# Kernel tuning notes

Measured on AMD Instinct MI355X. Metric: run time of the kernel, lower is better.

## Reference

```python
import jax, jax.numpy as jnp
import numpy as np

B, T, H = 8, 4096, 1024
K, V = 128, 128
OUT = 1024

def setup_inputs() -> dict:
    key = jax.random.key(0)
    k1, k2, k3, k4, k5 = jax.random.split(key, 5)
    s = 1.0 / np.sqrt(H)
    return {
        "hidden_state": jax.random.normal(k1, (B, T, H), dtype=jnp.float32),
        "W_proj": jax.random.normal(k2, (H, 3 * K + V), dtype=jnp.float32) * s,
        "b_proj": jax.random.normal(k3, (3 * K + V,), dtype=jnp.float32) * 0.01,
        "W_out": jax.random.normal(k4, (V, OUT), dtype=jnp.float32) * (1.0 / np.sqrt(V)),
        "b_out": jax.random.normal(k5, (OUT,), dtype=jnp.float32) * 0.01,
    }

def reference(hidden_state, W_proj, b_proj, W_out, b_out):
    # fused projection over all timesteps at once: (B,T,3K+V)
    qkgv = jnp.einsum("bth,hd->btd", hidden_state, W_proj) + b_proj
    q, k, g, v = jnp.split(qkgv, [K, 2 * K, 3 * K], axis=-1)
    k = jax.nn.sigmoid(k)
    g = jax.nn.sigmoid(g)

    # time-major for scan: (T,B,*)
    xs = (jnp.swapaxes(q, 0, 1), jnp.swapaxes(k, 0, 1),
          jnp.swapaxes(g, 0, 1), jnp.swapaxes(v, 0, 1))
    cell0 = jnp.zeros((B, K, V), dtype=hidden_state.dtype)

    def step(cell, x):
        q_i, k_i, g_i, v_i = x
        # gated outer-product state update: cell (B,K,V)
        cell = cell * g_i[:, :, None] + k_i[:, :, None] * v_i[:, None, :]
        # query readout: (B,V)
        o_i = jnp.einsum("bkv,bk->bv", cell, q_i)
        return cell, o_i

    final_state, outs = jax.lax.scan(step, cell0, xs)
    outputs = jnp.swapaxes(outs, 0, 1)  # (B,T,V)
    outputs = jnp.einsum("btv,vo->bto", outputs, W_out) + b_out
    return outputs, final_state
```

## Files before the change

### kernel.cpp

```cpp
#include <hip/hip_runtime.h>
#include <math.h>

#define B_ 8
#define T_ 4096
#define H_ 1024
#define K_ 128
#define V_ 128
#define OUT_ 1024
#define NPROJ 512
#define M_ (B_*T_)
#define CC 32
#define NC 128

typedef __attribute__((ext_vector_type(8))) short bf16x8;
typedef __attribute__((ext_vector_type(4))) float f32x4;

__device__ inline unsigned short f2bf(float f){
  union{float f; unsigned int u;} x; x.f = f;
  unsigned int r = x.u + 0x7fff + ((x.u>>16)&1);
  return (unsigned short)(r>>16);
}
__device__ inline float bf2f(unsigned short u){
  union{unsigned int i; float f;} x; x.i = ((unsigned int)u)<<16; return x.f;
}

#define GL16(gp, lp) __builtin_amdgcn_global_load_lds(\
  (const __attribute__((address_space(1))) unsigned int*)(gp), \
  (__attribute__((address_space(3))) unsigned int*)(lp), 16, 0, 0)

#define MFMA16(a,b,c) __builtin_amdgcn_mfma_f32_16x16x32_bf16((a),(b),(c),0,0,0)

__global__ __launch_bounds__(256)
void convT(const float* __restrict__ src, unsigned short* __restrict__ dst,
           int Kd, int N) {
  __shared__ float t[32][33];
  int tx = threadIdx.x & 31, ty = threadIdx.x >> 5;
  int n0 = blockIdx.x * 32, k0 = blockIdx.y * 32;
  #pragma unroll
  for (int r=0;r<4;r++){
    int k = ty*4 + r;
    t[k][tx] = src[(long)(k0+k)*N + n0 + tx];
  }
  __syncthreads();
  #pragma unroll
  for (int r=0;r<4;r++){
    int n = ty*4 + r;
    dst[(long)(n0+n)*Kd + k0 + tx] = f2bf(t[tx][n]);
  }
}

__global__ __launch_bounds__(512)
void proj_mfma3(const float* __restrict__ A, const unsigned short* __restrict__ Bt,
                const float* __restrict__ bias,
                unsigned short* __restrict__ qbf, unsigned short* __restrict__ kbf,
                float* __restrict__ gf, unsigned short* __restrict__ vbf) {
  __shared__ unsigned short sA[2][128*32];
  __shared__ unsigned short sB[2][256*32];
  int tid = threadIdx.x, lane = tid & 63, wid = tid >> 6;
  int wm = wid >> 2, wn = wid & 3;
  int l16 = lane & 15, g8 = (lane >> 4) * 8;
  long row0 = (long)blockIdx.y * 128;
  int col0 = blockIdx.x * 256;

  int arow = tid >> 2, akoff = (tid & 3) * 8;
  const float* Ab = A + (row0 + arow) * 1024 + akoff;
  int srow = lane >> 2, soff = (lane & 3) * 8;

  f32x4 acc[4][4];
  #pragma unroll
  for (int i=0;i<4;i++)
    #pragma unroll
    for (int j=0;j<4;j++) acc[i][j] = (f32x4){0.f,0.f,0.f,0.f};

  float4 ra0, ra1;
  #define LDA(k0_) { ra0 = *(const float4*)(Ab + (k0_)); ra1 = *(const float4*)(Ab + (k0_) + 4); }
  #define STB(b_, k0_) { _Pragma("unroll") \
    for (int i_=0;i_<2;i_++){ \
      int n0_ = wid*32 + i_*16; \
      GL16(Bt + (long)(col0 + n0_ + srow)*1024 + (k0_) + soff, &sB[b_][n0_*32]); \
    } }
  #define STA(b_) { \
    unsigned short o_[8] = {f2bf(ra0.x),f2bf(ra0.y),f2bf(ra0.z),f2bf(ra0.w), \
                            f2bf(ra1.x),f2bf(ra1.y),f2bf(ra1.z),f2bf(ra1.w)}; \
    *(uint4*)&sA[b_][arow*32 + akoff] = *(uint4*)o_; \
  }

  LDA(0);
  STB(0, 0);
  STA(0);
  __syncthreads();

  int cur = 0;
  for (int t = 0; t < 32; ++t) {
    int k0n = (t+1) * 32;
    if (t < 31) { LDA(k0n); STB(cur^1, k0n); }
    bf16x8 af[4], bf[4];
    #pragma unroll
    for (int mi=0;mi<4;mi++)
      af[mi] = *(const bf16x8*)&sA[cur][(wm*64 + mi*16 + l16)*32 + g8];
    #pragma unroll
    for (int ni=0;ni<4;ni++)
      bf[ni] = *(const bf16x8*)&sB[cur][(wn*64 + ni*16 + l16)*32 + g8];
    #pragma unroll
    for (int mi=0;mi<4;mi++)
      #pragma unroll
      for (int ni=0;ni<4;ni++)
        acc[mi][ni] = MFMA16(af[mi], bf[ni], acc[mi][ni]);
    if (t < 31) { STA(cur^1); }
    __syncthreads();
    cur ^= 1;
  }
  #undef LDA
  #undef STB
  #undef STA

  int seg = blockIdx.x*2 + (wn>>1);
  int cbase = (wn&1)*64;
  #pragma unroll
  for (int mi=0;mi<4;mi++){
    #pragma unroll
    for (int ni=0;ni<4;ni++){
      int c = cbase + ni*16 + l16;
      float bsv = bias[seg*128 + c];
      #pragma unroll
      for (int r=0;r<4;r++){
        long grow = row0 + wm*64 + mi*16 + (lane>>4)*4 + r;
        float v = acc[mi][ni][r] + bsv;
        long off = grow*128 + c;
        if (seg == 0)      qbf[off] = f2bf(v);
        else if (seg == 1) kbf[off] = f2bf(1.f/(1.f+__expf(-v)));
        else if (seg == 2) gf[off]  = 1.f/(1.f+__expf(-v));
        else               vbf[off] = f2bf(v);
      }
    }
  }
}

__global__ __launch_bounds__(128)
void prep(const float* __restrict__ gf, unsigned short* __restrict__ qbf,
          unsigned short* __restrict__ kbf, const unsigned short* __restrict__ vbf,
          unsigned short* __restrict__ khT, unsigned short* __restrict__ vT,
          float* __restrict__ Gc) {
  int k = threadIdx.x;
  int c = blockIdx.x, b = blockIdx.y;
  long base = ((long)b*T_ + (long)c*CC) * 128;
  float G = 1.f;
  float kt[CC];
  unsigned short vv[CC];
  #pragma unroll
  for (int t=0;t<CC;++t){
    long off = base + (long)t*128 + k;
    float g = gf[off];
    G *= g;
    float q = bf2f(qbf[off]);
    qbf[off] = f2bf(q*G);
    float kk = bf2f(kbf[off]);
    float ktl = kk/G;
    kbf[off] = f2bf(ktl);
    kt[t] = ktl;
    vv[t] = vbf[off];
  }
  long cb = (long)b*NC + c;
  Gc[cb*128 + k] = G;
  unsigned short ob[CC];
  #pragma unroll
  for (int s=0;s<CC;++s) ob[s] = f2bf(kt[s]*G);
  long tbase = (cb*128 + k)*CC;
  #pragma unroll
  for (int j=0;j<4;j++) *(uint4*)(khT + tbase + j*8) = *(uint4*)(ob + j*8);
  #pragma unroll
  for (int j=0;j<4;j++) *(uint4*)(vT + tbase + j*8) = *(uint4*)(vv + j*8);
}

__global__ __launch_bounds__(256)
void chunkstate(const unsigned short* __restrict__ khT, const unsigned short* __restrict__ vT,
                unsigned short* __restrict__ Ut) {
  __shared__ unsigned short kS[128][36];
  __shared__ unsigned short vS[128][36];
  int tid = threadIdx.x, lane = tid&63, w = tid>>6;
  long cb = (long)blockIdx.y*NC + blockIdx.x;
  const unsigned short* kg = khT + cb*4096;
  const unsigned short* vg = vT  + cb*4096;
  #pragma unroll
  for (int j=0;j<2;j++){
    int idx = tid + j*256;
    int r = idx>>2, s8 = (idx&3)*8;
    *(uint4*)&kS[r][s8] = *(const uint4*)(kg + r*32 + s8);
    *(uint4*)&vS[r][s8] = *(const uint4*)(vg + r*32 + s8);
  }
  __syncthreads();
  int l16 = lane&15, g8 = (lane>>4)*8;
  bf16x8 af[2], bfr[8];
  #pragma unroll
  for (int i=0;i<2;i++) af[i] = *(const bf16x8*)&vS[w*32 + i*16 + l16][g8];
  #pragma unroll
  for (int j=0;j<8;j++) bfr[j] = *(const bf16x8*)&kS[j*16 + l16][g8];
  #pragma unroll
  for (int i=0;i<2;i++){
    #pragma unroll
    for (int j=0;j<8;j++){
      f32x4 acc = (f32x4){0.f,0.f,0.f,0.f};
      acc = MFMA16(af[i], bfr[j], acc);
      int kcol = j*16 + l16;
      #pragma unroll
      for (int r=0;r<4;r++){
        int vrow = w*32 + i*16 + (lane>>4)*4 + r;
        Ut[cb*16384 + vrow*128 + kcol] = f2bf(acc[r]);
      }
    }
  }
}

__global__ __launch_bounds__(256)
void seqstate(const float* __restrict__ Gc, unsigned short* __restrict__ Ut,
              float* __restrict__ fstate) {
  int idx = blockIdx.x*256 + threadIdx.x;
  int b = blockIdx.y;
  int v = idx>>5, k0 = (idx&31)*4;
  float cell[4] = {0.f,0.f,0.f,0.f};
  long ub = (long)b*NC*16384 + (long)v*128 + k0;
  long gb = (long)b*NC*128 + k0;
  #pragma unroll 2
  for (int c=0; c<NC; ++c){
    uint2 u = *(const uint2*)(Ut + ub + (long)c*16384);
    float4 gc = *(const float4*)(Gc + gb + (long)c*128);
    unsigned short cb4[4] = {f2bf(cell[0]), f2bf(cell[1]), f2bf(cell[2]), f2bf(cell[3])};
    *(uint2*)(Ut + ub + (long)c*16384) = *(uint2*)cb4;
    cell[0] = fmaf(cell[0], gc.x, bf2f((unsigned short)(u.x & 0xffff)));
    cell[1] = fmaf(cell[1], gc.y, bf2f((unsigned short)(u.x >> 16)));
    cell[2] = fmaf(cell[2], gc.z, bf2f((unsigned short)(u.y & 0xffff)));
    cell[3] = fmaf(cell[3], gc.w, bf2f((unsigned short)(u.y >> 16)));
  }
  #pragma unroll
  for (int j=0;j<4;j++)
    fstate[((long)b*128 + k0 + j)*128 + v] = cell[j];
}

#define CP 140
__global__ __launch_bounds__(256)
void chunkout(const unsigned short* __restrict__ qbf, const unsigned short* __restrict__ kbf,
              const unsigned short* __restrict__ vT, const unsigned short* __restrict__ cellT,
              unsigned short* __restrict__ obf) {
  __shared__ unsigned short qS[32][CP];
  __shared__ unsigned short kS[32][CP];
  __shared__ unsigned short cS[128][CP];
  __shared__ unsigned short vS[128][36];
  __shared__ unsigned short pS[4][32][36];
  int tid = threadIdx.x, lane = tid&63, w = tid>>6;
  long cb = (long)blockIdx.y*NC + blockIdx.x;
  const unsigned short* qg = qbf + cb*4096;
  const unsigned short* kg = kbf + cb*4096;
  const unsigned short* vg = vT  + cb*4096;
  const unsigned short* cg = cellT + cb*16384;
  #pragma unroll
  for (int j=0;j<2;j++){
    int idx = tid + j*256;
    int r = idx>>4, c8 = (idx&15)*8;
    *(uint4*)&qS[r][c8] = *(const uint4*)(qg + r*128 + c8);
    *(uint4*)&kS[r][c8] = *(const uint4*)(kg + r*128 + c8);
    int rv = idx>>2, s8 = (idx&3)*8;
    *(uint4*)&vS[rv][s8] = *(const uint4*)(vg + rv*32 + s8);
  }
  #pragma unroll
  for (int j=0;j<8;j++){
    int idx = tid + j*256;
    int r = idx>>4, c8 = (idx&15)*8;
    *(uint4*)&cS[r][c8] = *(const uint4*)(cg + r*128 + c8);
  }
  __syncthreads();

  int l16 = lane&15, g = lane>>4, g8 = g*8;
  f32x4 s00 = (f32x4){0.f,0.f,0.f,0.f}, s01 = s00, s11 = s00;
  #pragma unroll
  for (int ks=0; ks<4; ++ks){
    bf16x8 ka = *(const bf16x8*)&kS[l16][ks*32+g8];
    bf16x8 kb = *(const bf16x8*)&kS[16+l16][ks*32+g8];
    bf16x8 qa = *(const bf16x8*)&qS[l16][ks*32+g8];
    bf16x8 qb = *(const bf16x8*)&qS[16+l16][ks*32+g8];
    s00 = MFMA16(ka, qa, s00);
    s01 = MFMA16(ka, qb, s01);
    s11 = MFMA16(kb, qb, s11);
  }
  pS[w][l16][16 + 4*g + (0)] = 0; pS[w][l16][16 + 4*g + 1] = 0;
  pS[w][l16][16 + 4*g + 2] = 0;   pS[w][l16][16 + 4*g + 3] = 0;
  #pragma unroll
  for (int r=0;r<4;r++){
    int sl = 4*g + r;
    pS[w][l16][sl]       = (l16 >= sl) ? f2bf(s00[r]) : (unsigned short)0;
    pS[w][16+l16][sl]    = f2bf(s01[r]);
    pS[w][16+l16][16+sl] = (l16 >= sl) ? f2bf(s11[r]) : (unsigned short)0;
  }
  f32x4 o[2][2];
  #pragma unroll
  for (int i=0;i<2;i++)
    #pragma unroll
    for (int j=0;j<2;j++) o[i][j] = (f32x4){0.f,0.f,0.f,0.f};
  {
    bf16x8 p0 = *(const bf16x8*)&pS[w][l16][g8];
    bf16x8 p1 = *(const bf16x8*)&pS[w][16+l16][g8];
    bf16x8 v0 = *(const bf16x8*)&vS[w*32 + l16][g8];
    bf16x8 v1 = *(const bf16x8*)&vS[w*32 + 16 + l16][g8];
    o[0][0] = MFMA16(p0, v0, o[0][0]);
    o[0][1] = MFMA16(p0, v1, o[0][1]);
    o[1][0] = MFMA16(p1, v0, o[1][0]);
    o[1][1] = MFMA16(p1, v1, o[1][1]);
  }
  #pragma unroll
  for (int ks=0; ks<4; ++ks){
    bf16x8 qa = *(const bf16x8*)&qS[l16][ks*32+g8];
    bf16x8 qb = *(const bf16x8*)&qS[16+l16][ks*32+g8];
    bf16x8 c0 = *(const bf16x8*)&cS[w*32 + l16][ks*32+g8];
    bf16x8 c1 = *(const bf16x8*)&cS[w*32 + 16 + l16][ks*32+g8];
    o[0][0] = MFMA16(qa, c0, o[0][0]);
    o[0][1] = MFMA16(qa, c1, o[0][1]);
    o[1][0] = MFMA16(qb, c0, o[1][0]);
    o[1][1] = MFMA16(qb, c1, o[1][1]);
  }
  #pragma unroll
  for (int ti=0;ti<2;ti++)
    #pragma unroll
    for (int vi=0;vi<2;vi++)
      #pragma unroll
      for (int r=0;r<4;r++){
        int t = ti*16 + 4*g + r;
        int v = w*32 + vi*16 + l16;
        obf[cb*4096 + (long)t*128 + v] = f2bf(o[ti][vi][r]);
      }
}

__global__ __launch_bounds__(256)
void out_mfma(const unsigned short* __restrict__ A, const unsigned short* __restrict__ Bt,
              const float* __restrict__ bias, float* __restrict__ C) {
  __shared__ unsigned short As[128*32];
  __shared__ unsigned short Bs[128*32];
  int tid = threadIdx.x, lane = tid & 63, wid = tid >> 6;
  long row0 = (long)blockIdx.y * 128;
  int col0 = blockIdx.x * 128;
  f32x4 acc[4][4];
  #pragma unroll
  for (int i=0;i<4;i++)
    #pragma unroll
    for (int j=0;j<4;j++) acc[i][j] = (f32x4){0.f,0.f,0.f,0.f};

  const unsigned short* Ab = A + row0*128;
  const unsigned short* Bb = Bt + (long)col0*128;
  int srow = lane >> 2;
  int soff = (lane & 3) * 8;
  int wrow = (wid>>1)*64, wcol = (wid&1)*64;

  for (int k0 = 0; k0 < 128; k0 += 32) {
    #pragma unroll
    for (int i=0;i<2;i++){
      int r = wid*32 + i*16;
      GL16(Ab + (long)(r + srow)*128 + k0 + soff, &As[r*32]);
      GL16(Bb + (long)(r + srow)*128 + k0 + soff, &Bs[r*32]);
    }
    __syncthreads();
    bf16x8 af[4], bfr[4];
    #pragma unroll
    for (int mi=0;mi<4;mi++)
      af[mi] = *(const bf16x8*)&As[(wrow + mi*16 + (lane&15))*32 + (lane>>4)*8];
    #pragma unroll
    for (int ni=0;ni<4;ni++)
      bfr[ni] = *(const bf16x8*)&Bs[(wcol + ni*16 + (lane&15))*32 + (lane>>4)*8];
    #pragma unroll
    for (int mi=0;mi<4;mi++)
      #pragma unroll
      for (int ni=0;ni<4;ni++)
        acc[mi][ni] = MFMA16(af[mi], bfr[ni], acc[mi][ni]);
    __syncthreads();
  }

  #pragma unroll
  for (int mi=0;mi<4;mi++){
    #pragma unroll
    for (int ni=0;ni<4;ni++){
      int col = col0 + wcol + ni*16 + (lane&15);
      float bsv = bias[col];
      #pragma unroll
      for (int r=0;r<4;r++){
        long grow = row0 + wrow + mi*16 + (lane>>4)*4 + r;
        C[grow*OUT_ + col] = acc[mi][ni][r] + bsv;
      }
    }
  }
}

extern "C" void kernel_launch(void* const* d_in, const int* in_sizes, int n_in,
                              void* d_out, int out_size, void* d_ws, size_t ws_size,
                              hipStream_t stream) {
  const float* hidden = (const float*)d_in[0];
  const float* Wp     = (const float*)d_in[1];
  const float* bp     = (const float*)d_in[2];
  const float* Wo     = (const float*)d_in[3];
  const float* bo     = (const float*)d_in[4];
  float* out    = (float*)d_out;
  float* fstate = out + (long)M_ * OUT_;

  char* w = (char*)d_ws;
  unsigned short* khT   = (unsigned short*)w;
  unsigned short* vT    = (unsigned short*)(w + 8388608);
  float*          Gc    = (float*)(w + 16777216);
  unsigned short* Ut    = (unsigned short*)(w + 17301504);
  unsigned short* obf   = (unsigned short*)(w + 50855936);
  unsigned short* Wot = (unsigned short*)(w + 67108864);
  unsigned short* Wpt = (unsigned short*)(w + 67371008);
  unsigned short* qbf = (unsigned short*)(w + 68419584);
  unsigned short* kbf = (unsigned short*)(w + 76808192);
  unsigned short* vbf = (unsigned short*)(w + 85196800);
  float*          gf  = (float*)(w + 93585408);

  convT<<<dim3(NPROJ/32, H_/32), 256, 0, stream>>>(Wp, Wpt, H_, NPROJ);
  convT<<<dim3(OUT_/32, V_/32), 256, 0, stream>>>(Wo, Wot, V_, OUT_);
  proj_mfma3<<<dim3(2, 256), 512, 0, stream>>>(hidden, Wpt, bp, qbf, kbf, gf, vbf);
  prep<<<dim3(NC, B_), 128, 0, stream>>>(gf, qbf, kbf, vbf, khT, vT, Gc);
  chunkstate<<<dim3(NC, B_), 256, 0, stream>>>(khT, vT, Ut);
  seqstate<<<dim3(16, B_), 256, 0, stream>>>(Gc, Ut, fstate);
  chunkout<<<dim3(NC, B_), 256, 0, stream>>>(qbf, kbf, vT, Ut, obf);
  out_mfma<<<dim3(8, 256), 256, 0, stream>>>(obf, Wot, bo, out);
}
```

Measured before the change: 194.3 us.

## Restructure projection GEMM: single-buffered 64-wide K tiles with padded/swizzled LDS

The projection GEMM drops LDS double buffering for a single buffer holding 64-wide K tiles, which halves the number of loop iterations and barriers. The A tile gets row padding (stride 72) and the B tile uses an XOR swizzle to avoid LDS bank conflicts. Launch bounds now request 4 waves per SIMD so that several blocks can share a CU. The cost is that there is less overlap between loads and compute within a block, because global loads now wait on two barriers per tile.

```diff
diff --git a/kernel.cpp b/kernel.cpp
--- a/kernel.cpp
+++ b/kernel.cpp
@@ -49,22 +49,23 @@
   }
 }
 
-__global__ __launch_bounds__(512)
-void proj_mfma3(const float* __restrict__ A, const unsigned short* __restrict__ Bt,
+__global__ __launch_bounds__(512, 4)
+void proj_mfma4(const float* __restrict__ A, const unsigned short* __restrict__ Bt,
                 const float* __restrict__ bias,
                 unsigned short* __restrict__ qbf, unsigned short* __restrict__ kbf,
                 float* __restrict__ gf, unsigned short* __restrict__ vbf) {
-  __shared__ unsigned short sA[2][128*32];
-  __shared__ unsigned short sB[2][256*32];
+  __shared__ unsigned short sA[128*72];
+  __shared__ unsigned short sB[256*64];
   int tid = threadIdx.x, lane = tid & 63, wid = tid >> 6;
   int wm = wid >> 2, wn = wid & 3;
   int l16 = lane & 15, g8 = (lane >> 4) * 8;
   long row0 = (long)blockIdx.y * 128;
   int col0 = blockIdx.x * 256;
 
-  int arow = tid >> 2, akoff = (tid & 3) * 8;
-  const float* Ab = A + (row0 + arow) * 1024 + akoff;
-  int srow = lane >> 2, soff = (lane & 3) * 8;
+  int arow = tid >> 2, acol0 = (tid & 3) * 16;
+  const float* Ab = A + (row0 + arow) * 1024 + acol0;
+  int srowB = lane >> 3;
+  int scolB = (((lane & 7) ^ (srowB & 7)) * 8);
 
   f32x4 acc[4][4];
   #pragma unroll
@@ -72,47 +73,55 @@
     #pragma unroll
     for (int j=0;j<4;j++) acc[i][j] = (f32x4){0.f,0.f,0.f,0.f};
 
-  float4 ra0, ra1;
-  #define LDA(k0_) { ra0 = *(const float4*)(Ab + (k0_)); ra1 = *(const float4*)(Ab + (k0_) + 4); }
-  #define STB(b_, k0_) { _Pragma("unroll") \
-    for (int i_=0;i_<2;i_++){ \
-      int n0_ = wid*32 + i_*16; \
-      GL16(Bt + (long)(col0 + n0_ + srow)*1024 + (k0_) + soff, &sB[b_][n0_*32]); \
+  float4 ra[4];
+  #define LDA(k0_) { _Pragma("unroll") \
+    for (int j_=0;j_<4;j_++) ra[j_] = *(const float4*)(Ab + (k0_) + j_*4); }
+  #define STA() { \
+    unsigned short o_[16]; \
+    _Pragma("unroll") \
+    for (int j_=0;j_<4;j_++){ \
+      o_[j_*4+0]=f2bf(ra[j_].x); o_[j_*4+1]=f2bf(ra[j_].y); \
+      o_[j_*4+2]=f2bf(ra[j_].z); o_[j_*4+3]=f2bf(ra[j_].w); \
+    } \
+    *(uint4*)&sA[arow*72 + acol0]     = ((uint4*)o_)[0]; \
+    *(uint4*)&sA[arow*72 + acol0 + 8] = ((uint4*)o_)[1]; \
+  }
+  #define STB(k0_) { _Pragma("unroll") \
+    for (int i_=0;i_<4;i_++){ \
+      int r_ = wid*32 + i_*8; \
+      GL16(Bt + (long)(col0 + r_ + srowB)*1024 + (k0_) + scolB, &sB[r_*64]); \
     } }
-  #define STA(b_) { \
-    unsigned short o_[8] = {f2bf(ra0.x),f2bf(ra0.y),f2bf(ra0.z),f2bf(ra0.w), \
-                            f2bf(ra1.x),f2bf(ra1.y),f2bf(ra1.z),f2bf(ra1.w)}; \
-    *(uint4*)&sA[b_][arow*32 + akoff] = *(uint4*)o_; \
-  }
 
   LDA(0);
-  STB(0, 0);
-  STA(0);
-  __syncthreads();
-
-  int cur = 0;
-  for (int t = 0; t < 32; ++t) {
-    int k0n = (t+1) * 32;
-    if (t < 31) { LDA(k0n); STB(cur^1, k0n); }
-    bf16x8 af[4], bf[4];
-    #pragma unroll
-    for (int mi=0;mi<4;mi++)
-      af[mi] = *(const bf16x8*)&sA[cur][(wm*64 + mi*16 + l16)*32 + g8];
-    #pragma unroll
-    for (int ni=0;ni<4;ni++)
-      bf[ni] = *(const bf16x8*)&sB[cur][(wn*64 + ni*16 + l16)*32 + g8];
-    #pragma unroll
-    for (int mi=0;mi<4;mi++)
-      #pragma unroll
-      for (int ni=0;ni<4;ni++)
-        acc[mi][ni] = MFMA16(af[mi], bf[ni], acc[mi][ni]);
-    if (t < 31) { STA(cur^1); }
+  for (int t = 0; t < 16; ++t) {
+    STA();
+    STB(t*64);
     __syncthreads();
-    cur ^= 1;
+    if (t < 15) { LDA(t*64 + 64); }
+    #pragma unroll
+    for (int kk2 = 0; kk2 < 2; ++kk2) {
+      int kk = kk2 * 32;
+      bf16x8 af[4], bf[4];
+      #pragma unroll
+      for (int mi=0;mi<4;mi++)
+        af[mi] = *(const bf16x8*)&sA[(wm*64 + mi*16 + l16)*72 + kk + g8];
+      #pragma unroll
+      for (int ni=0;ni<4;ni++){
+        int brow = wn*64 + ni*16 + l16;
+        int slot = ((kk + g8) >> 3) ^ (brow & 7);
+        bf[ni] = *(const bf16x8*)&sB[brow*64 + slot*8];
+      }
+      #pragma unroll
+      for (int mi=0;mi<4;mi++)
+        #pragma unroll
+        for (int ni=0;ni<4;ni++)
+          acc[mi][ni] = MFMA16(af[mi], bf[ni], acc[mi][ni]);
+    }
+    __syncthreads();
   }
   #undef LDA
+  #undef STA
   #undef STB
-  #undef STA
 
   int seg = blockIdx.x*2 + (wn>>1);
   int cbase = (wn&1)*64;
@@ -412,7 +421,7 @@
 
   convT<<<dim3(NPROJ/32, H_/32), 256, 0, stream>>>(Wp, Wpt, H_, NPROJ);
   convT<<<dim3(OUT_/32, V_/32), 256, 0, stream>>>(Wo, Wot, V_, OUT_);
-  proj_mfma3<<<dim3(2, 256), 512, 0, stream>>>(hidden, Wpt, bp, qbf, kbf, gf, vbf);
+  proj_mfma4<<<dim3(2, 256), 512, 0, stream>>>(hidden, Wpt, bp, qbf, kbf, gf, vbf);
   prep<<<dim3(NC, B_), 128, 0, stream>>>(gf, qbf, kbf, vbf, khT, vT, Gc);
   chunkstate<<<dim3(NC, B_), 256, 0, stream>>>(khT, vT, Ut);
   seqstate<<<dim3(16, B_), 256, 0, stream>>>(Gc, Ut, fstate);
```

Result: faster. 182.8 us (-5.9%).
